# Kernel tuning notes

Measured on AMD Instinct MI355X. Metric: run time of the kernel, lower is better.

Reference implementation:

```python
import jax, jax.numpy as jnp
import numpy as np

B, S, D = 512, 500, 128
NQ, NC, NQD, NCD = 10000, 500, 100, 100

def _glorot(key, shape):
    fan_in, fan_out = shape[0], shape[1]
    lim = np.sqrt(6.0 / (fan_in + fan_out))
    return jax.random.uniform(key, shape, jnp.float32, -lim, lim)

def setup_inputs() -> dict:
    key = jax.random.key(0)
    ks = jax.random.split(key, 24)
    inp = {
        'question_seq': jax.random.randint(ks[0], (B, S), 0, NQ),
        'concept_seq': jax.random.randint(ks[1], (B, S), 0, NC),
        'question_diff_seq': jax.random.randint(ks[2], (B, S), 0, NQD),
        'concept_diff_seq': jax.random.randint(ks[3], (B, S), 0, NCD),
        'correct_seq': jax.random.randint(ks[4], (B, S), 0, 2),
        # embedding tables
        'Eq': jax.random.normal(ks[5], (NQ, D), jnp.float32),
        'Ec': jax.random.normal(ks[6], (NC, D), jnp.float32),
        'Eqd': jax.random.normal(ks[7], (NQD, D), jnp.float32),
        'Ecd': jax.random.normal(ks[8], (NCD, D), jnp.float32),
        'Ecorr': jax.random.normal(ks[9], (2, D), jnp.float32),
        # linear layers (stored as [in, out], y = x @ W + b)
        'Wx': _glorot(ks[10], (4 * D, D)), 'bx': jnp.zeros((D,), jnp.float32),
        'Wsdf1': _glorot(ks[11], (D, D)), 'bsdf1': jnp.zeros((D,), jnp.float32),
        'Wsdf2': _glorot(ks[12], (D, D)), 'bsdf2': jnp.zeros((D,), jnp.float32),
        'Wpka1': _glorot(ks[13], (2 * D, D)), 'bpka1': jnp.zeros((D,), jnp.float32),
        'Wpka2': _glorot(ks[14], (2 * D, D)), 'bpka2': jnp.zeros((D,), jnp.float32),
        'Wki': _glorot(ks[15], (4 * D, D)), 'bki': jnp.zeros((D,), jnp.float32),
        # xavier_uniform init of h_pre (torch nn.init.xavier_uniform_ on zeros(B, D))
        'h0': _glorot(ks[16], (B, D)),
    }
    return inp

def reference(question_seq, concept_seq, question_diff_seq, concept_diff_seq,
              correct_seq, Eq, Ec, Eqd, Ecd, Ecorr, Wx, bx,
              Wsdf1, bsdf1, Wsdf2, bsdf2, Wpka1, bpka1, Wpka2, bpka2,
              Wki, bki, h0):
    # embed all sequences: [B, S, D]
    qe = Eq[question_seq]
    ce = Ec[concept_seq]
    qde = Eqd[question_diff_seq]
    cde = Ecd[concept_diff_seq]
    co = Ecorr[correct_seq]
    # x_t = generate_x_MLP(concat(...)) precomputed for all timesteps
    x_all = jnp.concatenate([qe, ce, qde, cde], axis=-1) @ Wx + bx  # [B, S, D]

    # time-major slices for scan over t = 0 .. S-2
    tm = lambda a: jnp.swapaxes(a, 0, 1)  # [S, B, D]
    xs = (tm(x_all)[:-1], tm(x_all)[1:], tm(co)[:-1], tm(qde)[:-1], tm(cde)[:-1])

    def step(h_pre, inputs):
        x_t, x_next, co_t, qd_t, cd_t = inputs
        input_sdf = x_t - h_pre
        sdf = jax.nn.sigmoid(input_sdf @ Wsdf1 + bsdf1) * jnp.tanh(input_sdf @ Wsdf2 + bsdf2)
        input_pka = jnp.concatenate([sdf, co_t], axis=-1)
        pka = jax.nn.sigmoid(input_pka @ Wpka1 + bpka1) * jnp.tanh(input_pka @ Wpka2 + bpka2)
        input_ki = jnp.concatenate([h_pre, co_t, qd_t, cd_t], axis=-1)
        gamma = jax.nn.sigmoid(input_ki @ Wki + bki)
        h = gamma * h_pre + (1.0 - gamma) * pka
        y_t = jax.nn.sigmoid(jnp.sum(x_next * h, axis=-1))  # [B]
        return h, y_t

    _, ys = jax.lax.scan(step, h0, xs)  # ys: [S-1, B]
    # y[:, S-1] is never written in the original (stays 0)
    y = jnp.concatenate([ys.T, jnp.zeros((question_seq.shape[0], 1), jnp.float32)], axis=1)
    return y
```

## Files before the change

### kernel.cpp

```cpp
#include <hip/hip_runtime.h>
#include <hip/hip_bf16.h>
#include <cstdint>
#include <cstddef>

#define BB 512
#define SS 500
#define TT 499
#define NRB 256
#define L2E 1.4426950408889634f

typedef float  f32x4  __attribute__((ext_vector_type(4)));
typedef short  bf16x8 __attribute__((ext_vector_type(8)));

#define MFMA16(A, B, C) __builtin_amdgcn_mfma_f32_16x16x32_bf16((A), (B), (C), 0, 0, 0)

static constexpr size_t OFF_TQ    = 0;
static constexpr size_t OFF_TC    = 10240000;
static constexpr size_t OFF_TQD   = 10752000;
static constexpr size_t OFF_TCD   = 10854400;
static constexpr size_t OFF_TCOK  = 10956800;
static constexpr size_t OFF_TP1   = 10957824;
static constexpr size_t OFF_TP2   = 10958848;
static constexpr size_t OFF_TMPA  = 10959872;
static constexpr size_t OFF_TMPB  = 11011072;
static constexpr size_t OFF_WFRAG = 11062272;
static constexpr size_t OFF_CPK   = 11226112;
static constexpr size_t OFF_STRM  = 11357184;
static constexpr size_t TOTAL_WS  = 142429184;

__device__ unsigned char g_fb[TOTAL_WS];

__device__ __forceinline__ unsigned short f2bf(float f) {
    union { float f; uint32_t u; } v; v.f = f;
    uint32_t u = v.u;
    uint32_t r = u + 0x7FFFu + ((u >> 16) & 1u);
    return (unsigned short)(r >> 16);
}
__device__ __forceinline__ float fsig(float z) {
    return __builtin_amdgcn_rcpf(1.0f + __expf(-z));
}
__device__ __forceinline__ float upk_x(uint32_t p) { return __uint_as_float(p & 0xffff0000u); }
__device__ __forceinline__ float upk_k(uint32_t p) { return __uint_as_float(p << 16); }
__device__ __forceinline__ uint32_t cvtpk(float lo, float hi) {
    uint32_t r;
    asm("v_cvt_pk_bf16_f32 %0, %1, %2" : "=v"(r) : "v"(lo), "v"(hi));
    return r;
}
__device__ __forceinline__ void bar_lgkm() {
    asm volatile("s_waitcnt lgkmcnt(0)" ::: "memory");
    __builtin_amdgcn_s_barrier();
}
__device__ __forceinline__ float sum16(float x) {
    int a = __float_as_int(x);
    int b = __builtin_amdgcn_update_dpp(a, a, 0xB1, 0xF, 0xF, false);
    float s = x + __int_as_float(b);
    int c = __float_as_int(s);
    int d = __builtin_amdgcn_update_dpp(c, c, 0x4E, 0xF, 0xF, false);
    s += __int_as_float(d);
    int e = __float_as_int(s);
    int f = __builtin_amdgcn_update_dpp(e, e, 0x141, 0xF, 0xF, false);
    s += __int_as_float(f);
    int gg = __float_as_int(s);
    int hh = __builtin_amdgcn_update_dpp(gg, gg, 0x140, 0xF, 0xF, false);
    return s + __int_as_float(hh);
}

__global__ __launch_bounds__(128) void k_tables(
    const float* __restrict__ Eq, const float* __restrict__ Ec,
    const float* __restrict__ Eqd, const float* __restrict__ Ecd,
    const float* __restrict__ Ecorr,
    const float* __restrict__ Wx,  const float* __restrict__ bx,
    const float* __restrict__ Wpka1, const float* __restrict__ bpka1,
    const float* __restrict__ Wpka2, const float* __restrict__ bpka2,
    const float* __restrict__ Wki, const float* __restrict__ bki,
    float* __restrict__ TQ, float* __restrict__ TC,
    float* __restrict__ TQD, float* __restrict__ TCD,
    float* __restrict__ TCOk, float* __restrict__ Tp1, float* __restrict__ Tp2,
    float* __restrict__ tmpA, float* __restrict__ tmpB)
{
    int blk = blockIdx.x;
    const float* A; const float* W; const float* bias = nullptr; float* out; int row;
    int ostride = 1;
    float oscale = 1.0f;
    if      (blk < 10000) { A = Eq;    row = blk;          W = Wx;              bias = bx;    out = TQ;   ostride = 2; }
    else if (blk < 10500) { A = Ec;    row = blk - 10000;  W = Wx  + 128*128;                 out = TC;   ostride = 2; }
    else if (blk < 10600) { A = Eqd;   row = blk - 10500;  W = Wx  + 256*128;                 out = TQD;  ostride = 2; }
    else if (blk < 10700) { A = Ecd;   row = blk - 10600;  W = Wx  + 384*128;                 out = TCD;  ostride = 2; }
    else if (blk < 10800) { A = Eqd;   row = blk - 10700;  W = Wki + 256*128;                 out = tmpA; }
    else if (blk < 10900) { A = Ecd;   row = blk - 10800;  W = Wki + 384*128;                 out = tmpB; }
    else if (blk < 10902) { A = Ecorr; row = blk - 10900;  W = Wki + 128*128;   bias = bki;   out = TCOk; oscale = -L2E; }
    else if (blk < 10904) { A = Ecorr; row = blk - 10902;  W = Wpka1 + 128*128; bias = bpka1; out = Tp1;  oscale = -L2E; }
    else                  { A = Ecorr; row = blk - 10904;  W = Wpka2 + 128*128; bias = bpka2; out = Tp2;  oscale = -2.0f*L2E; }

    __shared__ float a[128];
    int c = threadIdx.x;
    a[c] = A[row * 128 + c];
    __syncthreads();
    float acc = bias ? bias[c] : 0.0f;
    #pragma unroll 8
    for (int k = 0; k < 128; ++k) acc += a[k] * W[k * 128 + c];
    out[(size_t)(row * 128 + c) * ostride] = acc * oscale;
}

__global__ __launch_bounds__(128) void k_tables2(
    const float* __restrict__ Wki,
    float* __restrict__ TQ, float* __restrict__ TC,
    float* __restrict__ TQD, float* __restrict__ TCD,
    const float* __restrict__ tmpA, const float* __restrict__ tmpB)
{
    int blk = blockIdx.x;
    float* base2; const float* tmp = nullptr; int row;
    if      (blk < 10000) { row = blk;          base2 = TQ  + (size_t)row * 256; }
    else if (blk < 10500) { row = blk - 10000;  base2 = TC  + (size_t)row * 256; }
    else if (blk < 10600) { row = blk - 10500;  base2 = TQD + (size_t)row * 256; tmp = tmpA + (size_t)row * 128; }
    else                  { row = blk - 10600;  base2 = TCD + (size_t)row * 256; tmp = tmpB + (size_t)row * 128; }
    __shared__ float a[128];
    int c = threadIdx.x;
    a[c] = base2[c * 2];
    __syncthreads();
    float acc = tmp ? tmp[c] : 0.0f;
    #pragma unroll 8
    for (int k = 0; k < 128; ++k) acc += a[k] * Wki[k * 128 + c];
    base2[c * 2 + 1] = acc * (-L2E);
}

__global__ __launch_bounds__(64) void k_wfrag(
    const float* __restrict__ Wsdf1, const float* __restrict__ Wsdf2,
    const float* __restrict__ Wpka1, const float* __restrict__ Wpka2,
    const float* __restrict__ Wki, unsigned short* __restrict__ wfrag)
{
    int bid = blockIdx.x;
    int m = bid >> 5, w = (bid >> 2) & 7, kt = bid & 3;
    const float* W = (m == 0) ? Wsdf1 : (m == 1) ? Wsdf2 : (m == 2) ? Wpka1 : (m == 3) ? Wpka2 : Wki;
    float sgn = (m == 0) ? -L2E : (m == 1) ? -2.0f*L2E : (m == 2) ? -L2E : (m == 3) ? -2.0f*L2E : L2E;
    int l = threadIdx.x;
    int cc = w * 16 + (l & 15);
    int k0 = kt * 32 + ((l >> 4) << 3);
    unsigned short v[8];
    #pragma unroll
    for (int j = 0; j < 8; ++j) v[j] = f2bf(sgn * W[(size_t)(k0 + j) * 128 + cc]);
    unsigned short* dst = wfrag + ((( (size_t)m * 8 + w) * 4 + kt) * 64 + l) * 8;
    #pragma unroll
    for (int j = 0; j < 8; ++j) dst[j] = v[j];
}

__global__ __launch_bounds__(512) void k_gather(
    const int* __restrict__ qs, const int* __restrict__ cs,
    const int* __restrict__ qds, const int* __restrict__ cds, const int* __restrict__ corr,
    const float2* __restrict__ TQ, const float2* __restrict__ TC,
    const float2* __restrict__ TQD, const float2* __restrict__ TCD,
    const float* __restrict__ TCOk,
    uint32_t* __restrict__ strm, unsigned char* __restrict__ cpk)
{
    int bid = blockIdx.x;
    int t = bid >> 7, chunk = bid & 127;
    int tid = threadIdx.x;
    int b = chunk * 4 + (tid >> 7);
    int col = tid & 127;

    int iq  = qs  [(size_t)b * SS + t];
    int ic  = cs  [(size_t)b * SS + t];
    int iqd = qds [(size_t)b * SS + t];
    int icd = cds [(size_t)b * SS + t];
    int ico = corr[(size_t)b * SS + t];

    float2 q  = TQ [(size_t)iq  * 128 + col];
    float2 c_ = TC [(size_t)ic  * 128 + col];
    float2 qd = TQD[(size_t)iqd * 128 + col];
    float2 cd = TCD[(size_t)icd * 128 + col];
    float  co = TCOk[(size_t)ico * 128 + col];

    float xs = q.x + c_.x + qd.x + cd.x;
    float ks = q.y + c_.y + qd.y + cd.y + co;
    strm[((size_t)t * BB + b) * 128 + col] = cvtpk(ks, xs);

    if (tid < 2) {
        int rb = chunk * 2 + tid;
        unsigned char bpk = (unsigned char)((corr[(size_t)(rb * 2) * SS + t] & 1)
                          | ((corr[(size_t)(rb * 2 + 1) * SS + t] & 1) << 1));
        cpk[(size_t)rb * 512 + t] = bpk;
    }
}

__global__ __launch_bounds__(512, 2) void k_rec(
    const uint32_t* __restrict__ strm, const unsigned char* __restrict__ cpkg,
    const unsigned short* __restrict__ wfrag,
    const float* __restrict__ Tp1, const float* __restrict__ Tp2,
    const float* __restrict__ bsdf1, const float* __restrict__ bsdf2,
    const float* __restrict__ h0, float* __restrict__ y)
{
    int rb = blockIdx.x;
    int tid = threadIdx.x;
    int w = tid >> 6, l = tid & 63;
    int g = l >> 4, cl = l & 15;
    int col = w * 16 + cl;
    int row = g & 1;
    bool owner = (g < 2);

    __shared__ __align__(16) unsigned short dbuf[256];
    __shared__ __align__(16) unsigned short sbuf[256];
    __shared__ __align__(16) float ybuf[2][2][8];

    bf16x8 wf[5][4];
    #pragma unroll
    for (int m = 0; m < 5; ++m)
        #pragma unroll
        for (int kt = 0; kt < 4; ++kt)
            wf[m][kt] = *(const bf16x8*)(wfrag + ((((size_t)m * 8 + w) * 4 + kt) * 64 + l) * 8);

    float bs1 = bsdf1[col] * (-L2E);
    float bs2 = bsdf2[col] * (-2.0f * L2E);
    float tp1a = Tp1[col], tp1b = Tp1[128 + col];
    float tp2a = Tp2[col], tp2b = Tp2[128 + col];

    float h = h0[(size_t)(rb * 2 + row) * 128 + col];

    char* pdw = (char*)dbuf + row * 256 + ((col * 2) ^ (row << 6));
    char* psw = (char*)sbuf + row * 256 + ((col * 2) ^ (row << 6));
    const bf16x8* prd[4]; const bf16x8* prs[4];
    int rrow = cl & 1;
    #pragma unroll
    for (int kt = 0; kt < 4; ++kt) {
        int off = rrow * 256 + ((kt * 64 + g * 16) ^ (rrow << 6));
        prd[kt] = (const bf16x8*)((char*)dbuf + off);
        prs[kt] = (const bf16x8*)((char*)sbuf + off);
    }

    const size_t TSTR = (size_t)BB * 128;
    const uint32_t* sp = strm + (size_t)(rb * 2 + row) * 128 + col;
    const unsigned char* cp = cpkg + (size_t)rb * 512;

    float* yrow = y + (size_t)(rb * 2) * SS;

    float kip_c; unsigned int c_c;
    {
        uint32_t p0 = sp[0];
        kip_c = upk_k(p0);
        c_c = (cp[0] >> row) & 1u;
        float x0 = upk_x(p0);
        uint32_t pk = cvtpk(x0 - h, x0 - h);
        if (owner) *(unsigned short*)pdw = (unsigned short)pk;
    }
    bar_lgkm();

    #pragma unroll 2
    for (int t = 0; t < TT; ++t) {
        uint32_t pkN = sp[(size_t)(t + 1) * TSTR];
        unsigned char cN = cp[t + 1];

        f32x4 s1a = {bs1, bs1, bs1, bs1}, s1b = {0.f, 0.f, 0.f, 0.f};
        f32x4 s2a = {bs2, bs2, bs2, bs2}, s2b = {0.f, 0.f, 0.f, 0.f};
        f32x4 gda = {kip_c, kip_c, kip_c, kip_c}, gdb = {0.f, 0.f, 0.f, 0.f};
        {
            bf16x8 d0 = *prd[0], d1 = *prd[1], d2 = *prd[2], d3 = *prd[3];
            s1a = MFMA16(d0, wf[0][0], s1a); s2a = MFMA16(d0, wf[1][0], s2a); gda = MFMA16(d0, wf[4][0], gda);
            s1b = MFMA16(d2, wf[0][2], s1b); s2b = MFMA16(d2, wf[1][2], s2b); gdb = MFMA16(d2, wf[4][2], gdb);
            s1a = MFMA16(d1, wf[0][1], s1a); s2a = MFMA16(d1, wf[1][1], s2a); gda = MFMA16(d1, wf[4][1], gda);
            s1b = MFMA16(d3, wf[0][3], s1b); s2b = MFMA16(d3, wf[1][3], s2b); gdb = MFMA16(d3, wf[4][3], gdb);
        }
        float s1v = (row ? s1a[1] : s1a[0]) + (row ? s1b[1] : s1b[0]);
        float s2v = (row ? s2a[1] : s2a[0]) + (row ? s2b[1] : s2b[0]);
        float gdv = (row ? gda[1] : gda[0]) + (row ? gdb[1] : gdb[0]);
        float gv = __builtin_amdgcn_rcpf(1.0f + __builtin_amdgcn_exp2f(gdv));
        float e1 = __builtin_amdgcn_exp2f(s1v), e2 = __builtin_amdgcn_exp2f(s2v);
        float sdf = (1.0f - e2) * __builtin_amdgcn_rcpf((1.0f + e1) * (1.0f + e2));
        {
            uint32_t pk = cvtpk(sdf, sdf);
            if (owner) *(unsigned short*)psw = (unsigned short)pk;
        }
        bar_lgkm();

        if (t > 0 && w == 0 && l < 2) {
            const float* yb = ybuf[(t - 1) & 1][l];
            float s = (yb[0] + yb[1]) + (yb[2] + yb[3]) + (yb[4] + yb[5]) + (yb[6] + yb[7]);
            yrow[(size_t)l * SS + (t - 1)] = fsig(s);
        }

        f32x4 p1a = {0.f, 0.f, 0.f, 0.f}, p1b = {0.f, 0.f, 0.f, 0.f};
        f32x4 p2a = {0.f, 0.f, 0.f, 0.f}, p2b = {0.f, 0.f, 0.f, 0.f};
        {
            bf16x8 f0 = *prs[0], f1 = *prs[1], f2 = *prs[2], f3 = *prs[3];
            p1a = MFMA16(f0, wf[2][0], p1a); p2a = MFMA16(f0, wf[3][0], p2a);
            p1b = MFMA16(f2, wf[2][2], p1b); p2b = MFMA16(f2, wf[3][2], p2b);
            p1a = MFMA16(f1, wf[2][1], p1a); p2a = MFMA16(f1, wf[3][1], p2a);
            p1b = MFMA16(f3, wf[2][3], p1b); p2b = MFMA16(f3, wf[3][3], p2b);
        }
        float p1v = (row ? p1a[1] : p1a[0]) + (row ? p1b[1] : p1b[0]);
        float p2v = (row ? p2a[1] : p2a[0]) + (row ? p2b[1] : p2b[0]);
        float t1 = c_c ? tp1b : tp1a;
        float t2 = c_c ? tp2b : tp2a;
        float e1p = __builtin_amdgcn_exp2f(p1v + t1), e2p = __builtin_amdgcn_exp2f(p2v + t2);
        float pka = (1.0f - e2p) * __builtin_amdgcn_rcpf((1.0f + e1p) * (1.0f + e2p));
        h = gv * (h - pka) + pka;

        float xn = upk_x(pkN);
        {
            uint32_t pk = cvtpk(xn - h, xn - h);
            if (owner) *(unsigned short*)pdw = (unsigned short)pk;
        }
        float yv = sum16(xn * h);
        if (owner && cl == 0) ybuf[t & 1][row][w] = yv;
        bar_lgkm();

        kip_c = upk_k(pkN);
        c_c = ((unsigned int)cN >> row) & 1u;
    }

    if (w == 0 && l < 2) {
        const float* yb = ybuf[(TT - 1) & 1][l];
        float s = (yb[0] + yb[1]) + (yb[2] + yb[3]) + (yb[4] + yb[5]) + (yb[6] + yb[7]);
        yrow[(size_t)l * SS + (TT - 1)] = fsig(s);
        yrow[(size_t)l * SS + TT] = 0.0f;
    }
}

extern "C" void kernel_launch(void* const* d_in, const int* in_sizes, int n_in,
                              void* d_out, int out_size, void* d_ws, size_t ws_size,
                              hipStream_t stream) {
    const int* qs    = (const int*)d_in[0];
    const int* cs    = (const int*)d_in[1];
    const int* qds   = (const int*)d_in[2];
    const int* cds   = (const int*)d_in[3];
    const int* corr  = (const int*)d_in[4];
    const float* Eq    = (const float*)d_in[5];
    const float* Ec    = (const float*)d_in[6];
    const float* Eqd   = (const float*)d_in[7];
    const float* Ecd   = (const float*)d_in[8];
    const float* Ecorr = (const float*)d_in[9];
    const float* Wx    = (const float*)d_in[10];
    const float* bx    = (const float*)d_in[11];
    const float* Wsdf1 = (const float*)d_in[12];
    const float* bsdf1 = (const float*)d_in[13];
    const float* Wsdf2 = (const float*)d_in[14];
    const float* bsdf2 = (const float*)d_in[15];
    const float* Wpka1 = (const float*)d_in[16];
    const float* bpka1 = (const float*)d_in[17];
    const float* Wpka2 = (const float*)d_in[18];
    const float* bpka2 = (const float*)d_in[19];
    const float* Wki   = (const float*)d_in[20];
    const float* bki   = (const float*)d_in[21];
    const float* h0    = (const float*)d_in[22];

    char* base;
    if (ws_size >= TOTAL_WS) {
        base = (char*)d_ws;
    } else {
        void* p = nullptr;
        hipGetSymbolAddress(&p, HIP_SYMBOL(g_fb));
        base = (char*)p;
    }

    float* TQ    = (float*)(base + OFF_TQ);
    float* TC    = (float*)(base + OFF_TC);
    float* TQD   = (float*)(base + OFF_TQD);
    float* TCD   = (float*)(base + OFF_TCD);
    float* TCOk  = (float*)(base + OFF_TCOK);
    float* Tp1   = (float*)(base + OFF_TP1);
    float* Tp2   = (float*)(base + OFF_TP2);
    float* tmpA  = (float*)(base + OFF_TMPA);
    float* tmpB  = (float*)(base + OFF_TMPB);
    unsigned short* wfrag = (unsigned short*)(base + OFF_WFRAG);
    unsigned char*  cpk   = (unsigned char*)(base + OFF_CPK);
    uint32_t* strm = (uint32_t*)(base + OFF_STRM);

    k_tables<<<10906, 128, 0, stream>>>(Eq, Ec, Eqd, Ecd, Ecorr, Wx, bx,
                                        Wpka1, bpka1, Wpka2, bpka2, Wki, bki,
                                        TQ, TC, TQD, TCD, TCOk, Tp1, Tp2, tmpA, tmpB);
    k_tables2<<<10700, 128, 0, stream>>>(Wki, TQ, TC, TQD, TCD, tmpA, tmpB);
    k_wfrag<<<160, 64, 0, stream>>>(Wsdf1, Wsdf2, Wpka1, Wpka2, Wki, wfrag);
    k_gather<<<SS * 128, 512, 0, stream>>>(qs, cs, qds, cds, corr,
                                           (const float2*)TQ, (const float2*)TC,
                                           (const float2*)TQD, (const float2*)TCD, TCOk,
                                           strm, cpk);
    k_rec<<<NRB, 512, 0, stream>>>(strm, cpk, wfrag, Tp1, Tp2,
                                   bsdf1, bsdf2, h0, (float*)d_out);
}
```

Baseline: 502.4 us.

## Fold Wx·Wki into combined weights and tile table precompute over 16 rows

Precomputes combined weight matrices Wx_m·Wki (plus the Wki diff-slices) and the projected bias, so each embedding row's Wki projection is obtained directly from the embedding in one pass instead of a second dependent kernel. The table kernel now processes 16 rows per block, reusing each weight load across rows held in shared memory and writing both outputs as float2. This removes one launch of over ten thousand blocks and cuts redundant weight reads, at the cost of a small extra combine kernel and slightly different floating-point rounding order.

```diff
diff --git a/kernel.cpp b/kernel.cpp
--- a/kernel.cpp
+++ b/kernel.cpp
@@ -21,12 +21,12 @@
 static constexpr size_t OFF_TCOK  = 10956800;
 static constexpr size_t OFF_TP1   = 10957824;
 static constexpr size_t OFF_TP2   = 10958848;
-static constexpr size_t OFF_TMPA  = 10959872;
-static constexpr size_t OFF_TMPB  = 11011072;
-static constexpr size_t OFF_WFRAG = 11062272;
-static constexpr size_t OFF_CPK   = 11226112;
-static constexpr size_t OFF_STRM  = 11357184;
-static constexpr size_t TOTAL_WS  = 142429184;
+static constexpr size_t OFF_WCOMB = 10959872;
+static constexpr size_t OFF_BKQ   = 11222016;
+static constexpr size_t OFF_WFRAG = 11223040;
+static constexpr size_t OFF_CPK   = 11386880;
+static constexpr size_t OFF_STRM  = 11517952;
+static constexpr size_t TOTAL_WS  = 142589952;
 
 __device__ unsigned char g_fb[TOTAL_WS];
 
@@ -65,6 +65,34 @@
     return s + __int_as_float(hh);
 }
 
+__global__ __launch_bounds__(128) void k_wcomb(
+    const float* __restrict__ Wx, const float* __restrict__ bx,
+    const float* __restrict__ Wki,
+    float* __restrict__ Wcomb, float* __restrict__ bkq)
+{
+    int blk = blockIdx.x;
+    int c = threadIdx.x;
+    __shared__ float a[128];
+    float acc;
+    if (blk < 512) {
+        int m = blk >> 7, r = blk & 127;
+        a[c] = Wx[(size_t)(m * 128 + r) * 128 + c];
+        acc = (m == 2) ? Wki[(size_t)(256 + r) * 128 + c]
+            : (m == 3) ? Wki[(size_t)(384 + r) * 128 + c] : 0.0f;
+        __syncthreads();
+        #pragma unroll 8
+        for (int k = 0; k < 128; ++k) acc += a[k] * Wki[k * 128 + c];
+        Wcomb[(size_t)(m * 128 + (blk & 127)) * 128 + c] = acc;
+    } else {
+        a[c] = bx[c];
+        acc = 0.0f;
+        __syncthreads();
+        #pragma unroll 8
+        for (int k = 0; k < 128; ++k) acc += a[k] * Wki[k * 128 + c];
+        bkq[c] = acc;
+    }
+}
+
 __global__ __launch_bounds__(128) void k_tables(
     const float* __restrict__ Eq, const float* __restrict__ Ec,
     const float* __restrict__ Eqd, const float* __restrict__ Ecd,
@@ -73,55 +101,69 @@
     const float* __restrict__ Wpka1, const float* __restrict__ bpka1,
     const float* __restrict__ Wpka2, const float* __restrict__ bpka2,
     const float* __restrict__ Wki, const float* __restrict__ bki,
-    float* __restrict__ TQ, float* __restrict__ TC,
-    float* __restrict__ TQD, float* __restrict__ TCD,
-    float* __restrict__ TCOk, float* __restrict__ Tp1, float* __restrict__ Tp2,
-    float* __restrict__ tmpA, float* __restrict__ tmpB)
+    const float* __restrict__ Wcomb, const float* __restrict__ bkq,
+    float2* __restrict__ TQ, float2* __restrict__ TC,
+    float2* __restrict__ TQD, float2* __restrict__ TCD,
+    float* __restrict__ TCOk, float* __restrict__ Tp1, float* __restrict__ Tp2)
 {
     int blk = blockIdx.x;
-    const float* A; const float* W; const float* bias = nullptr; float* out; int row;
-    int ostride = 1;
-    float oscale = 1.0f;
-    if      (blk < 10000) { A = Eq;    row = blk;          W = Wx;              bias = bx;    out = TQ;   ostride = 2; }
-    else if (blk < 10500) { A = Ec;    row = blk - 10000;  W = Wx  + 128*128;                 out = TC;   ostride = 2; }
-    else if (blk < 10600) { A = Eqd;   row = blk - 10500;  W = Wx  + 256*128;                 out = TQD;  ostride = 2; }
-    else if (blk < 10700) { A = Ecd;   row = blk - 10600;  W = Wx  + 384*128;                 out = TCD;  ostride = 2; }
-    else if (blk < 10800) { A = Eqd;   row = blk - 10700;  W = Wki + 256*128;                 out = tmpA; }
-    else if (blk < 10900) { A = Ecd;   row = blk - 10800;  W = Wki + 384*128;                 out = tmpB; }
-    else if (blk < 10902) { A = Ecorr; row = blk - 10900;  W = Wki + 128*128;   bias = bki;   out = TCOk; oscale = -L2E; }
-    else if (blk < 10904) { A = Ecorr; row = blk - 10902;  W = Wpka1 + 128*128; bias = bpka1; out = Tp1;  oscale = -L2E; }
-    else                  { A = Ecorr; row = blk - 10904;  W = Wpka2 + 128*128; bias = bpka2; out = Tp2;  oscale = -2.0f*L2E; }
-
-    __shared__ float a[128];
     int c = threadIdx.x;
-    a[c] = A[row * 128 + c];
+
+    if (blk >= 671) {
+        int s = blk - 671;
+        int row = s & 1;
+        const float* W; const float* bias; float* out; float osc;
+        if      (s < 2) { W = Wki   + 128*128; bias = bki;   out = TCOk; osc = -L2E; }
+        else if (s < 4) { W = Wpka1 + 128*128; bias = bpka1; out = Tp1;  osc = -L2E; }
+        else            { W = Wpka2 + 128*128; bias = bpka2; out = Tp2;  osc = -2.0f*L2E; }
+        __shared__ float a2[128];
+        a2[c] = Ecorr[row * 128 + c];
+        __syncthreads();
+        float acc = bias[c];
+        #pragma unroll 8
+        for (int k = 0; k < 128; ++k) acc += a2[k] * W[k * 128 + c];
+        out[row * 128 + c] = acc * osc;
+        return;
+    }
+
+    const float* A; float2* out; int row0, nrows, m;
+    if      (blk < 625) { m = 0; A = Eq;  out = TQ;  row0 = blk * 16;          nrows = 16; }
+    else if (blk < 657) { m = 1; A = Ec;  out = TC;  row0 = (blk - 625) * 16;  nrows = (row0 + 16 <= 500) ? 16 : 500 - row0; }
+    else if (blk < 664) { m = 2; A = Eqd; out = TQD; row0 = (blk - 657) * 16;  nrows = (row0 + 16 <= 100) ? 16 : 100 - row0; }
+    else                { m = 3; A = Ecd; out = TCD; row0 = (blk - 664) * 16;  nrows = (row0 + 16 <= 100) ? 16 : 100 - row0; }
+
+    const float* Wxp = Wx + (size_t)m * 128 * 128;
+    const float* Wkp = Wcomb + (size_t)m * 128 * 128;
+
+    __shared__ float as[16][128];
+    #pragma unroll
+    for (int r = 0; r < 16; ++r)
+        as[r][c] = (r < nrows) ? A[(size_t)(row0 + r) * 128 + c] : 0.0f;
     __syncthreads();
-    float acc = bias ? bias[c] : 0.0f;
-    #pragma unroll 8
-    for (int k = 0; k < 128; ++k) acc += a[k] * W[k * 128 + c];
-    out[(size_t)(row * 128 + c) * ostride] = acc * oscale;
-}
-
-__global__ __launch_bounds__(128) void k_tables2(
-    const float* __restrict__ Wki,
-    float* __restrict__ TQ, float* __restrict__ TC,
-    float* __restrict__ TQD, float* __restrict__ TCD,
-    const float* __restrict__ tmpA, const float* __restrict__ tmpB)
-{
-    int blk = blockIdx.x;
-    float* base2; const float* tmp = nullptr; int row;
-    if      (blk < 10000) { row = blk;          base2 = TQ  + (size_t)row * 256; }
-    else if (blk < 10500) { row = blk - 10000;  base2 = TC  + (size_t)row * 256; }
-    else if (blk < 10600) { row = blk - 10500;  base2 = TQD + (size_t)row * 256; tmp = tmpA + (size_t)row * 128; }
-    else                  { row = blk - 10600;  base2 = TCD + (size_t)row * 256; tmp = tmpB + (size_t)row * 128; }
-    __shared__ float a[128];
-    int c = threadIdx.x;
-    a[c] = base2[c * 2];
-    __syncthreads();
-    float acc = tmp ? tmp[c] : 0.0f;
-    #pragma unroll 8
-    for (int k = 0; k < 128; ++k) acc += a[k] * Wki[k * 128 + c];
-    base2[c * 2 + 1] = acc * (-L2E);
+
+    float accx[16], acck[16];
+    float bx0 = (m == 0) ? bx[c] : 0.0f;
+    float bk0 = (m == 0) ? bkq[c] : 0.0f;
+    #pragma unroll
+    for (int r = 0; r < 16; ++r) { accx[r] = bx0; acck[r] = bk0; }
+
+    #pragma unroll 2
+    for (int k = 0; k < 128; ++k) {
+        float wx = Wxp[k * 128 + c];
+        float wk = Wkp[k * 128 + c];
+        #pragma unroll
+        for (int r = 0; r < 16; ++r) {
+            accx[r] += as[r][k] * wx;
+            acck[r] += as[r][k] * wk;
+        }
+    }
+    #pragma unroll
+    for (int r = 0; r < 16; ++r) {
+        if (r < nrows) {
+            float2 o; o.x = accx[r]; o.y = acck[r] * (-L2E);
+            out[(size_t)(row0 + r) * 128 + c] = o;
+        }
+    }
 }
 
 __global__ __launch_bounds__(64) void k_wfrag(
@@ -350,23 +392,23 @@
         base = (char*)p;
     }
 
-    float* TQ    = (float*)(base + OFF_TQ);
-    float* TC    = (float*)(base + OFF_TC);
-    float* TQD   = (float*)(base + OFF_TQD);
-    float* TCD   = (float*)(base + OFF_TCD);
+    float2* TQ   = (float2*)(base + OFF_TQ);
+    float2* TC   = (float2*)(base + OFF_TC);
+    float2* TQD  = (float2*)(base + OFF_TQD);
+    float2* TCD  = (float2*)(base + OFF_TCD);
     float* TCOk  = (float*)(base + OFF_TCOK);
     float* Tp1   = (float*)(base + OFF_TP1);
     float* Tp2   = (float*)(base + OFF_TP2);
-    float* tmpA  = (float*)(base + OFF_TMPA);
-    float* tmpB  = (float*)(base + OFF_TMPB);
+    float* Wcomb = (float*)(base + OFF_WCOMB);
+    float* bkq   = (float*)(base + OFF_BKQ);
     unsigned short* wfrag = (unsigned short*)(base + OFF_WFRAG);
     unsigned char*  cpk   = (unsigned char*)(base + OFF_CPK);
     uint32_t* strm = (uint32_t*)(base + OFF_STRM);
 
-    k_tables<<<10906, 128, 0, stream>>>(Eq, Ec, Eqd, Ecd, Ecorr, Wx, bx,
-                                        Wpka1, bpka1, Wpka2, bpka2, Wki, bki,
-                                        TQ, TC, TQD, TCD, TCOk, Tp1, Tp2, tmpA, tmpB);
-    k_tables2<<<10700, 128, 0, stream>>>(Wki, TQ, TC, TQD, TCD, tmpA, tmpB);
+    k_wcomb<<<513, 128, 0, stream>>>(Wx, bx, Wki, Wcomb, bkq);
+    k_tables<<<677, 128, 0, stream>>>(Eq, Ec, Eqd, Ecd, Ecorr, Wx, bx,
+                                      Wpka1, bpka1, Wpka2, bpka2, Wki, bki,
+                                      Wcomb, bkq, TQ, TC, TQD, TCD, TCOk, Tp1, Tp2);
     k_wfrag<<<160, 64, 0, stream>>>(Wsdf1, Wsdf2, Wpka1, Wpka2, Wki, wfrag);
     k_gather<<<SS * 128, 512, 0, stream>>>(qs, cs, qds, cds, corr,
                                            (const float2*)TQ, (const float2*)TC,
```

New measurement: 496.5 us. Within noise of the previous version (-1.2%).
